# Kernel tuning notes

Measured on AMD Instinct MI355X. Metric: run time of the kernel, lower is better.

## Reference

```python
import jax, jax.numpy as jnp
import numpy as np

N_RAYS = 32768
N_SAMPLES = N_RAYS * 32  # 1,048,576
FDIM = 32
HID = 64
RGB_HID = 64
THRESHOLD = 1e-4  # early_termination_threshold


def setup_inputs() -> dict:
    key = jax.random.key(0)
    ks = jax.random.split(key, 12)
    # ragged per-ray sample counts (avg 32), adjusted so total is exactly N_SAMPLES
    rng = np.random.default_rng(0)
    counts = rng.integers(8, 57, size=N_RAYS)
    delta = int(N_SAMPLES - counts.sum())
    if delta >= 0:
        counts[:delta] += 1
    else:
        counts[:(-delta)] -= 1
    starts = np.concatenate([[0], np.cumsum(counts)[:-1]])
    packing_info = jnp.asarray(np.stack([starts, counts], axis=1), dtype=jnp.int32)
    ray_ids = jnp.asarray(np.repeat(np.arange(N_RAYS), counts), dtype=jnp.int32)

    pos = jax.random.uniform(ks[0], (N_SAMPLES, 3), minval=-1.0, maxval=1.0)
    dirs = jax.random.normal(ks[1], (N_SAMPLES, 3))
    dirs = dirs / jnp.linalg.norm(dirs, axis=1, keepdims=True)
    dt = jax.random.uniform(ks[2], (N_SAMPLES, 1), minval=0.0, maxval=0.01)
    packed_samples = jnp.concatenate([pos, dirs, dt], axis=1)

    def lin(k, fi, fo):
        return jax.random.normal(k, (fi, fo)) / np.sqrt(fi)

    return {
        "packed_samples": packed_samples,
        "packing_info": packing_info,
        "ray_ids": ray_ids,
        "w1": lin(ks[3], 3, HID), "b1": jnp.zeros(HID),
        "w2": lin(ks[4], HID, FDIM), "b2": jnp.zeros(FDIM),
        "w_sigma": lin(ks[5], FDIM, 1), "b_sigma": jnp.zeros(1),
        "w_rgb1": lin(ks[6], FDIM + 3, RGB_HID), "b_rgb1": jnp.zeros(RGB_HID),
        "w_rgb2": lin(ks[7], RGB_HID, 3), "b_rgb2": jnp.zeros(3),
        "bg_color": jnp.ones(3),
    }


def reference(packed_samples, packing_info, ray_ids, w1, b1, w2, b2,
              w_sigma, b_sigma, w_rgb1, b_rgb1, w_rgb2, b_rgb2, bg_color):
    pos = packed_samples[:, :3]
    dirs = packed_samples[:, 3:6]
    dt = packed_samples[:, 6]

    # feature_module
    feats = jax.nn.relu(pos @ w1 + b1) @ w2 + b2            # [N, FDIM]
    # sigma_decoder
    sigma = jax.nn.softplus(feats @ w_sigma + b_sigma)[:, 0]  # [N]

    # NerfWeights: per-ray transmittance T_i = exp(-sum_{j<i in ray} sigma_j*dt_j),
    # weight_i = T_i * (1 - exp(-sigma_i*dt_i)), zeroed once T drops below threshold.
    tau = sigma * dt
    c_excl = jnp.cumsum(tau) - tau                           # exclusive global cumsum
    seg_base = c_excl[packing_info[:, 0]]                    # cumsum before each ray's start
    T = jnp.exp(-(c_excl - seg_base[ray_ids]))
    alpha = 1.0 - jnp.exp(-tau)
    weights = jnp.where(T > THRESHOLD, T * alpha, 0.0)       # [N]

    # rgb_decoder (masked gather in torch is a perf trick; weight==0 kills masked rgbs)
    h = jax.nn.relu(jnp.concatenate([feats, dirs], axis=1) @ w_rgb1 + b_rgb1)
    rgbs = jax.nn.sigmoid(h @ w_rgb2 + b_rgb2)               # [N, 3]

    contrib = rgbs * weights[:, None]
    rendered = jax.ops.segment_sum(contrib, ray_ids, num_segments=N_RAYS)   # [n_rays,3]
    opac = jax.ops.segment_sum(weights, ray_ids, num_segments=N_RAYS)       # [n_rays]
    return rendered + bg_color * (1.0 - opac[:, None])
```

## Files before the change

kernel.cpp:

```cpp
#include <hip/hip_runtime.h>
#include <hip/hip_bf16.h>
#include <math.h>
#include <stdint.h>

#define N_RAYS    32768
#define N_SAMPLES (N_RAYS * 32)
#define N_TILES   (N_SAMPLES / 32)
#define THRESH 0.0001f
#define TBL_OFF  (16u * 1024u * 1024u)

#define R_A1   0
#define R_A2   2
#define R_R1A  6
#define R_R1B  10
#define R_AR2  12
#define R_AR2F 16
#define R_B2I  18
#define R_ARI  22
#define NREC   26

#define NWAVES 3072
#define NITER  11

typedef __attribute__((ext_vector_type(8)))  __bf16 bf16x8;
typedef __attribute__((ext_vector_type(16))) float  f32x16;
typedef float f4a __attribute__((ext_vector_type(4), aligned(4)));

union FragU  { __hip_bfloat162 h2[4]; uint32_t w[4]; bf16x8 v; };
union RecU   { bf16x8 v; uint4 u; };
union Rec16U { f32x16 v; uint4 u[4]; float f[16]; };

__device__ inline __hip_bfloat162 pk2(float lo, float hi) {
    float2 t; t.x = lo; t.y = hi;
    return __float22bfloat162_rn(t);
}

__device__ inline bf16x8 pack8(const float* vals) {
    FragU u;
    u.h2[0] = pk2(vals[0], vals[1]);
    u.h2[1] = pk2(vals[2], vals[3]);
    u.h2[2] = pk2(vals[4], vals[5]);
    u.h2[3] = pk2(vals[6], vals[7]);
    return u.v;
}

__device__ inline float rcp_fast(float x) {
    float r;
    asm("v_rcp_f32 %0, %1" : "=v"(r) : "v"(x));
    return r;
}
__device__ inline float sigmoid_fast(float x) { return rcp_fast(1.0f + __expf(-x)); }
__device__ inline float softplus_fast(float x) {
    const float e = __expf(-fabsf(x));
    return fmaxf(x, 0.0f) + __logf(1.0f + e);
}

template <int P>
__device__ inline bf16x8 packB_relu(f32x16 a) {
    FragU u;
    u.h2[0] = pk2(fmaxf(a[P+0],0.f), fmaxf(a[P+1],0.f));
    u.h2[1] = pk2(fmaxf(a[P+2],0.f), fmaxf(a[P+3],0.f));
    u.h2[2] = pk2(fmaxf(a[P+4],0.f), fmaxf(a[P+5],0.f));
    u.h2[3] = pk2(fmaxf(a[P+6],0.f), fmaxf(a[P+7],0.f));
    return u.v;
}
template <int P>
__device__ inline bf16x8 packB_relu2(f32x16 x, f32x16 y) {
    FragU u;
    u.h2[0] = pk2(fmaxf(x[P+0]+y[P+0],0.f), fmaxf(x[P+1]+y[P+1],0.f));
    u.h2[1] = pk2(fmaxf(x[P+2]+y[P+2],0.f), fmaxf(x[P+3]+y[P+3],0.f));
    u.h2[2] = pk2(fmaxf(x[P+4]+y[P+4],0.f), fmaxf(x[P+5]+y[P+5],0.f));
    u.h2[3] = pk2(fmaxf(x[P+6]+y[P+6],0.f), fmaxf(x[P+7]+y[P+7],0.f));
    return u.v;
}
template <int P>
__device__ inline bf16x8 packB_plain2(f32x16 x, f32x16 y) {
    FragU u;
    u.h2[0] = pk2(x[P+0]+y[P+0], x[P+1]+y[P+1]);
    u.h2[1] = pk2(x[P+2]+y[P+2], x[P+3]+y[P+3]);
    u.h2[2] = pk2(x[P+4]+y[P+4], x[P+5]+y[P+5]);
    u.h2[3] = pk2(x[P+6]+y[P+6], x[P+7]+y[P+7]);
    return u.v;
}

__global__ __launch_bounds__(256) void nerf_build_frags(
    const float* __restrict__ w1,  const float* __restrict__ b1,
    const float* __restrict__ w2,  const float* __restrict__ b2,
    const float* __restrict__ w_sigma, const float* __restrict__ b_sigma,
    const float* __restrict__ w_rgb1,  const float* __restrict__ b_rgb1,
    const float* __restrict__ w_rgb2,  const float* __restrict__ b_rgb2,
    uint4* __restrict__ tbl)
{
    const int wid  = threadIdx.x >> 6;
    const int lane = threadIdx.x & 63;
    const int m    = lane & 31;
    const int h    = lane >> 5;
    RecU rec;

    if (wid == 0) {
        #pragma unroll
        for (int t = 0; t < 2; ++t) {
            float v[8] = {0,0,0,0,0,0,0,0};
            if (h == 0) {
                const int j = 32*t + m;
                v[0] = w1[j]; v[1] = w1[64+j]; v[2] = w1[128+j]; v[3] = b1[j];
            }
            rec.v = pack8(v); tbl[(R_A1+t)*64 + lane] = rec.u;
        }
        #pragma unroll
        for (int c = 0; c < 4; ++c) {
            float v[8];
            #pragma unroll
            for (int q = 0; q < 8; ++q) {
                const int j = 16*c + (q&3) + 8*(q>>2) + 4*h;
                v[q] = w2[j*32 + m];
            }
            rec.v = pack8(v); tbl[(R_A2+c)*64 + lane] = rec.u;
        }
    } else if (wid == 1) {
        #pragma unroll
        for (int t = 0; t < 2; ++t)
            #pragma unroll
            for (int c = 0; c < 2; ++c) {
                float v[8];
                #pragma unroll
                for (int q = 0; q < 8; ++q) {
                    const int f = 16*c + (q&3) + 8*(q>>2) + 4*h;
                    v[q] = w_rgb1[f*64 + 32*t + m];
                }
                rec.v = pack8(v); tbl[(R_R1A+2*t+c)*64 + lane] = rec.u;
            }
        #pragma unroll
        for (int t = 0; t < 2; ++t) {
            float v[8] = {0,0,0,0,0,0,0,0};
            if (h == 1) {
                const int j = 32*t + m;
                v[0] = w_rgb1[32*64 + j]; v[1] = w_rgb1[33*64 + j];
                v[2] = w_rgb1[34*64 + j]; v[3] = b_rgb1[j];
            }
            rec.v = pack8(v); tbl[(R_R1B+t)*64 + lane] = rec.u;
        }
    } else if (wid == 2) {
        #pragma unroll
        for (int c = 0; c < 4; ++c) {
            float v[8];
            #pragma unroll
            for (int q = 0; q < 8; ++q) {
                const int hh = 16*c + (q&3) + 8*(q>>2) + 4*h;
                v[q] = (m < 3) ? w_rgb2[hh*3 + m] : 0.0f;
            }
            rec.v = pack8(v); tbl[(R_AR2+c)*64 + lane] = rec.u;
        }
        #pragma unroll
        for (int c = 0; c < 2; ++c) {
            float v[8];
            #pragma unroll
            for (int q = 0; q < 8; ++q) {
                const int f = 16*c + (q&3) + 8*(q>>2) + 4*h;
                v[q] = (m == 3) ? w_sigma[f] : 0.0f;
            }
            rec.v = pack8(v); tbl[(R_AR2F+c)*64 + lane] = rec.u;
        }
        Rec16U r16;
        #pragma unroll
        for (int i = 0; i < 4; ++i) {
            #pragma unroll
            for (int e = 0; e < 4; ++e) r16.f[4*i+e] = b2[e + 8*i + 4*h];
        }
        #pragma unroll
        for (int i = 0; i < 4; ++i) tbl[(R_B2I+i)*64 + lane] = r16.u[i];
        #pragma unroll
        for (int i = 0; i < 4; ++i) {
            #pragma unroll
            for (int e = 0; e < 4; ++e) {
                const int r = e + 8*i + 4*h;
                r16.f[4*i+e] = (r < 3) ? b_rgb2[r] : ((r == 3) ? b_sigma[0] : 0.0f);
            }
        }
        #pragma unroll
        for (int i = 0; i < 4; ++i) tbl[(R_ARI+i)*64 + lane] = r16.u[i];
    }
}

__global__ __launch_bounds__(256, 3) void nerf_mlp_mfma(
    const float* __restrict__ samples,
    const uint4* __restrict__ tbl,
    float4* __restrict__ out)
{
    __shared__ uint4 wlds[NREC * 64];

    for (int i = threadIdx.x; i < NREC * 64; i += 256) wlds[i] = tbl[i];
    __syncthreads();

    const int lane = threadIdx.x & 63;
    const int m32  = lane & 31;
    const int h    = lane >> 5;
    const int wgid = (blockIdx.x * blockDim.x + threadIdx.x) >> 6;

    const uint4* wl = &wlds[lane];
    #define LDW(rec) ({ RecU r_; r_.u = wl[(rec)*64]; r_.v; })

    f4a sa[2], sb[2];
    {
        const float* sp = samples + (size_t)(wgid * 32 + m32) * 7;
        sa[0] = *(const f4a*)sp;  sb[0] = *(const f4a*)(sp + 3);
    }

    const f32x16 zero16 = {0,0,0,0,0,0,0,0,0,0,0,0,0,0,0,0};

    #pragma unroll
    for (int u = 0; u < NITER; ++u) {
        const int cb = u & 1;
        const int nb = (u + 1) & 1;
        const int t  = wgid + u * NWAVES;
        if (u < NITER - 1) {
            int tn = wgid + (u + 1) * NWAVES;
            if (tn > N_TILES - 1) tn = N_TILES - 1;
            const float* sp = samples + (size_t)(tn * 32 + m32) * 7;
            sa[nb] = *(const f4a*)sp;  sb[nb] = *(const f4a*)(sp + 3);
        }

        FragU bin;
        bin.h2[0] = pk2(h ? sb[cb].x : sa[cb].x, h ? sb[cb].y : sa[cb].y);
        bin.h2[1] = pk2(h ? sb[cb].z : sa[cb].z, 1.0f);
        bin.w[2] = 0; bin.w[3] = 0;

        bf16x8 B2c[4];
        {
            f32x16 a0 = __builtin_amdgcn_mfma_f32_32x32x16_bf16(LDW(R_A1+0), bin.v, zero16, 0,0,0);
            f32x16 a1 = __builtin_amdgcn_mfma_f32_32x32x16_bf16(LDW(R_A1+1), bin.v, zero16, 0,0,0);
            B2c[0] = packB_relu<0>(a0);
            B2c[1] = packB_relu<8>(a0);
            B2c[2] = packB_relu<0>(a1);
            B2c[3] = packB_relu<8>(a1);
        }

        bf16x8 Bf0, Bf1;
        {
            Rec16U rc;
            #pragma unroll
            for (int i = 0; i < 4; ++i) rc.u[i] = wl[(R_B2I+i)*64];
            f32x16 u0, u1;
            u0 = __builtin_amdgcn_mfma_f32_32x32x16_bf16(LDW(R_A2+0), B2c[0], rc.v, 0,0,0);
            u1 = __builtin_amdgcn_mfma_f32_32x32x16_bf16(LDW(R_A2+2), B2c[2], zero16, 0,0,0);
            u0 = __builtin_amdgcn_mfma_f32_32x32x16_bf16(LDW(R_A2+1), B2c[1], u0, 0,0,0);
            u1 = __builtin_amdgcn_mfma_f32_32x32x16_bf16(LDW(R_A2+3), B2c[3], u1, 0,0,0);
            Bf0 = packB_plain2<0>(u0, u1);
            Bf1 = packB_plain2<8>(u0, u1);
        }

        bf16x8 Bh[4];
        {
            f32x16 p0, p1, q0, q1;
            q0 = __builtin_amdgcn_mfma_f32_32x32x16_bf16(LDW(R_R1B+0), bin.v, zero16, 0,0,0);
            q1 = __builtin_amdgcn_mfma_f32_32x32x16_bf16(LDW(R_R1B+1), bin.v, zero16, 0,0,0);
            p0 = __builtin_amdgcn_mfma_f32_32x32x16_bf16(LDW(R_R1A+0), Bf0, zero16, 0,0,0);
            p1 = __builtin_amdgcn_mfma_f32_32x32x16_bf16(LDW(R_R1A+2), Bf0, zero16, 0,0,0);
            p0 = __builtin_amdgcn_mfma_f32_32x32x16_bf16(LDW(R_R1A+1), Bf1, p0, 0,0,0);
            p1 = __builtin_amdgcn_mfma_f32_32x32x16_bf16(LDW(R_R1A+3), Bf1, p1, 0,0,0);
            Bh[0] = packB_relu2<0>(p0, q0);
            Bh[1] = packB_relu2<8>(p0, q0);
            Bh[2] = packB_relu2<0>(p1, q1);
            Bh[3] = packB_relu2<8>(p1, q1);
        }

        float ar0, ar1, ar2, ar3;
        {
            Rec16U rc;
            #pragma unroll
            for (int i = 0; i < 4; ++i) rc.u[i] = wl[(R_ARI+i)*64];
            f32x16 x, y, z;
            x = __builtin_amdgcn_mfma_f32_32x32x16_bf16(LDW(R_AR2F+0), Bf0, rc.v, 0,0,0);
            y = __builtin_amdgcn_mfma_f32_32x32x16_bf16(LDW(R_AR2+0), Bh[0], zero16, 0,0,0);
            z = __builtin_amdgcn_mfma_f32_32x32x16_bf16(LDW(R_AR2+2), Bh[2], zero16, 0,0,0);
            x = __builtin_amdgcn_mfma_f32_32x32x16_bf16(LDW(R_AR2F+1), Bf1, x, 0,0,0);
            y = __builtin_amdgcn_mfma_f32_32x32x16_bf16(LDW(R_AR2+1), Bh[1], y, 0,0,0);
            z = __builtin_amdgcn_mfma_f32_32x32x16_bf16(LDW(R_AR2+3), Bh[3], z, 0,0,0);
            ar0 = x[0] + y[0] + z[0];
            ar1 = x[1] + y[1] + z[1];
            ar2 = x[2] + y[2] + z[2];
            ar3 = x[3] + y[3] + z[3];
        }

        const float rr    = sigmoid_fast(ar0);
        const float gg    = sigmoid_fast(ar1);
        const float bb    = sigmoid_fast(ar2);
        const float sigma = softplus_fast(ar3);
        const float tau   = sigma * sb[cb].w;
        if (t < N_TILES && lane < 32)
            out[t * 32 + m32] = make_float4(tau, rr, gg, bb);
    }
    #undef LDW
}

__global__ __launch_bounds__(256) void nerf_render_kernel(
    const float4* __restrict__ smp,
    const int*    __restrict__ packing,
    const float*  __restrict__ bg,
    float*        __restrict__ out)
{
    const int gtid = blockIdx.x * blockDim.x + threadIdx.x;
    const int ray  = gtid >> 6;
    const int lane = threadIdx.x & 63;
    if (ray >= N_RAYS) return;

    const int start = packing[2 * ray];
    const int count = packing[2 * ray + 1];

    float tau = 0.0f, r = 0.0f, g = 0.0f, b = 0.0f;
    if (lane < count) {
        const float4 v = smp[start + lane];
        tau = v.x; r = v.y; g = v.z; b = v.w;
    }

    float incl = tau;
    #pragma unroll
    for (int off = 1; off < 64; off <<= 1) {
        const float v = __shfl_up(incl, off, 64);
        if (lane >= off) incl += v;
    }
    const float c_excl = incl - tau;

    const float T     = __expf(-c_excl);
    const float alpha = 1.0f - __expf(-tau);
    float w = (lane < count && T > THRESH) ? T * alpha : 0.0f;

    float cr = r * w, cg = g * w, cb = b * w;

    #pragma unroll
    for (int off = 32; off > 0; off >>= 1) {
        cr += __shfl_down(cr, off, 64);
        cg += __shfl_down(cg, off, 64);
        cb += __shfl_down(cb, off, 64);
        w  += __shfl_down(w,  off, 64);
    }

    if (lane == 0) {
        out[ray * 3 + 0] = cr + bg[0] * (1.0f - w);
        out[ray * 3 + 1] = cg + bg[1] * (1.0f - w);
        out[ray * 3 + 2] = cb + bg[2] * (1.0f - w);
    }
}

extern "C" void kernel_launch(void* const* d_in, const int* in_sizes, int n_in,
                              void* d_out, int out_size, void* d_ws, size_t ws_size,
                              hipStream_t stream) {
    const float* samples  = (const float*)d_in[0];
    const int*   packing  = (const int*)  d_in[1];
    const float* w1       = (const float*)d_in[3];
    const float* b1       = (const float*)d_in[4];
    const float* w2       = (const float*)d_in[5];
    const float* b2       = (const float*)d_in[6];
    const float* w_sigma  = (const float*)d_in[7];
    const float* b_sigma  = (const float*)d_in[8];
    const float* w_rgb1   = (const float*)d_in[9];
    const float* b_rgb1   = (const float*)d_in[10];
    const float* w_rgb2   = (const float*)d_in[11];
    const float* b_rgb2   = (const float*)d_in[12];
    const float* bg       = (const float*)d_in[13];

    float4* smp = (float4*)d_ws;
    uint4*  tbl = (uint4*)((char*)d_ws + TBL_OFF);
    float*  out = (float*)d_out;

    nerf_build_frags<<<1, 256, 0, stream>>>(
        w1, b1, w2, b2, w_sigma, b_sigma,
        w_rgb1, b_rgb1, w_rgb2, b_rgb2, tbl);

    nerf_mlp_mfma<<<768, 256, 0, stream>>>(samples, tbl, (float4*)smp);

    nerf_render_kernel<<<(N_RAYS * 64) / 256, 256, 0, stream>>>(smp, packing, bg, out);
}
```

Before: 49.92 us.

## Fuse MLP and volume rendering into one kernel with ray-grouped blocks

Merges the MFMA MLP kernel and the render kernel into a single kernel where each block handles 8 consecutive rays. It evaluates the MLP on their packed samples and keeps tau/rgb in LDS before the per-ray scan and reduction. This removes the 16 MB intermediate write/read through global memory and one kernel launch. In exchange it drops the persistent-wave software prefetch and the 3-wave occupancy hint, and relies on 8 rays never exceeding 464 samples. Blocks also now do ragged tile counts, which can leave some waves idle.

New measurement: 70.62 us. 41.5% more time.

```diff
diff --git a/kernel.cpp b/kernel.cpp
--- a/kernel.cpp
+++ b/kernel.cpp
@@ -5,9 +5,9 @@
 
 #define N_RAYS    32768
 #define N_SAMPLES (N_RAYS * 32)
-#define N_TILES   (N_SAMPLES / 32)
 #define THRESH 0.0001f
-#define TBL_OFF  (16u * 1024u * 1024u)
+#define RPB    8
+#define MAXS   464
 
 #define R_A1   0
 #define R_A2   2
@@ -18,9 +18,6 @@
 #define R_B2I  18
 #define R_ARI  22
 #define NREC   26
-
-#define NWAVES 3072
-#define NITER  11
 
 typedef __attribute__((ext_vector_type(8)))  __bf16 bf16x8;
 typedef __attribute__((ext_vector_type(16))) float  f32x16;
@@ -182,47 +179,47 @@
     }
 }
 
-__global__ __launch_bounds__(256, 3) void nerf_mlp_mfma(
+__global__ __launch_bounds__(256) void nerf_fused(
     const float* __restrict__ samples,
+    const int*   __restrict__ packing,
     const uint4* __restrict__ tbl,
-    float4* __restrict__ out)
+    const float* __restrict__ bg,
+    float*       __restrict__ out)
 {
-    __shared__ uint4 wlds[NREC * 64];
+    __shared__ uint4  wlds[NREC * 64];
+    __shared__ float4 obuf[MAXS];
 
     for (int i = threadIdx.x; i < NREC * 64; i += 256) wlds[i] = tbl[i];
-    __syncthreads();
 
     const int lane = threadIdx.x & 63;
     const int m32  = lane & 31;
     const int h    = lane >> 5;
-    const int wgid = (blockIdx.x * blockDim.x + threadIdx.x) >> 6;
+    const int wid  = threadIdx.x >> 6;
+    const int ray0 = blockIdx.x * RPB;
+
+    const int start0 = packing[2 * ray0];
+    int total = 0;
+    #pragma unroll
+    for (int i = 0; i < RPB; ++i) total += packing[2 * (ray0 + i) + 1];
+
+    __syncthreads();
 
     const uint4* wl = &wlds[lane];
     #define LDW(rec) ({ RecU r_; r_.u = wl[(rec)*64]; r_.v; })
 
-    f4a sa[2], sb[2];
-    {
-        const float* sp = samples + (size_t)(wgid * 32 + m32) * 7;
-        sa[0] = *(const f4a*)sp;  sb[0] = *(const f4a*)(sp + 3);
-    }
-
     const f32x16 zero16 = {0,0,0,0,0,0,0,0,0,0,0,0,0,0,0,0};
-
-    #pragma unroll
-    for (int u = 0; u < NITER; ++u) {
-        const int cb = u & 1;
-        const int nb = (u + 1) & 1;
-        const int t  = wgid + u * NWAVES;
-        if (u < NITER - 1) {
-            int tn = wgid + (u + 1) * NWAVES;
-            if (tn > N_TILES - 1) tn = N_TILES - 1;
-            const float* sp = samples + (size_t)(tn * 32 + m32) * 7;
-            sa[nb] = *(const f4a*)sp;  sb[nb] = *(const f4a*)(sp + 3);
-        }
+    const int ntiles = (total + 31) >> 5;
+
+    for (int t = wid; t < ntiles; t += 4) {
+        const int sidx  = 32 * t + m32;
+        const int cl    = (sidx < total) ? sidx : (total - 1);
+        const float* sp = samples + (size_t)(start0 + cl) * 7;
+        const f4a sa = *(const f4a*)sp;
+        const f4a sb = *(const f4a*)(sp + 3);
 
         FragU bin;
-        bin.h2[0] = pk2(h ? sb[cb].x : sa[cb].x, h ? sb[cb].y : sa[cb].y);
-        bin.h2[1] = pk2(h ? sb[cb].z : sa[cb].z, 1.0f);
+        bin.h2[0] = pk2(h ? sb.x : sa.x, h ? sb.y : sa.y);
+        bin.h2[1] = pk2(h ? sb.z : sa.z, 1.0f);
         bin.w[2] = 0; bin.w[3] = 0;
 
         bf16x8 B2c[4];
@@ -286,59 +283,53 @@
         const float gg    = sigmoid_fast(ar1);
         const float bb    = sigmoid_fast(ar2);
         const float sigma = softplus_fast(ar3);
-        const float tau   = sigma * sb[cb].w;
-        if (t < N_TILES && lane < 32)
-            out[t * 32 + m32] = make_float4(tau, rr, gg, bb);
+        const float tau   = sigma * sb.w;
+        if (lane < 32 && sidx < total)
+            obuf[sidx] = make_float4(tau, rr, gg, bb);
     }
     #undef LDW
-}
-
-__global__ __launch_bounds__(256) void nerf_render_kernel(
-    const float4* __restrict__ smp,
-    const int*    __restrict__ packing,
-    const float*  __restrict__ bg,
-    float*        __restrict__ out)
-{
-    const int gtid = blockIdx.x * blockDim.x + threadIdx.x;
-    const int ray  = gtid >> 6;
-    const int lane = threadIdx.x & 63;
-    if (ray >= N_RAYS) return;
-
-    const int start = packing[2 * ray];
-    const int count = packing[2 * ray + 1];
-
-    float tau = 0.0f, r = 0.0f, g = 0.0f, b = 0.0f;
-    if (lane < count) {
-        const float4 v = smp[start + lane];
-        tau = v.x; r = v.y; g = v.z; b = v.w;
-    }
-
-    float incl = tau;
+
+    __syncthreads();
+
+    const float bg0 = bg[0], bg1 = bg[1], bg2 = bg[2];
     #pragma unroll
-    for (int off = 1; off < 64; off <<= 1) {
-        const float v = __shfl_up(incl, off, 64);
-        if (lane >= off) incl += v;
-    }
-    const float c_excl = incl - tau;
-
-    const float T     = __expf(-c_excl);
-    const float alpha = 1.0f - __expf(-tau);
-    float w = (lane < count && T > THRESH) ? T * alpha : 0.0f;
-
-    float cr = r * w, cg = g * w, cb = b * w;
-
-    #pragma unroll
-    for (int off = 32; off > 0; off >>= 1) {
-        cr += __shfl_down(cr, off, 64);
-        cg += __shfl_down(cg, off, 64);
-        cb += __shfl_down(cb, off, 64);
-        w  += __shfl_down(w,  off, 64);
-    }
-
-    if (lane == 0) {
-        out[ray * 3 + 0] = cr + bg[0] * (1.0f - w);
-        out[ray * 3 + 1] = cg + bg[1] * (1.0f - w);
-        out[ray * 3 + 2] = cb + bg[2] * (1.0f - w);
+    for (int ri = 0; ri < 2; ++ri) {
+        const int ray   = ray0 + wid * 2 + ri;
+        const int rs    = packing[2 * ray] - start0;
+        const int count = packing[2 * ray + 1];
+
+        float tau = 0.0f, r = 0.0f, g = 0.0f, b = 0.0f;
+        if (lane < count) {
+            const float4 v = obuf[rs + lane];
+            tau = v.x; r = v.y; g = v.z; b = v.w;
+        }
+
+        float incl = tau;
+        #pragma unroll
+        for (int off = 1; off < 64; off <<= 1) {
+            const float v = __shfl_up(incl, off, 64);
+            if (lane >= off) incl += v;
+        }
+        const float c_excl = incl - tau;
+
+        const float T     = __expf(-c_excl);
+        const float alpha = 1.0f - __expf(-tau);
+        float w = (lane < count && T > THRESH) ? T * alpha : 0.0f;
+
+        float cr = r * w, cg = g * w, cb = b * w;
+        #pragma unroll
+        for (int off = 32; off > 0; off >>= 1) {
+            cr += __shfl_down(cr, off, 64);
+            cg += __shfl_down(cg, off, 64);
+            cb += __shfl_down(cb, off, 64);
+            w  += __shfl_down(w,  off, 64);
+        }
+
+        if (lane == 0) {
+            out[ray * 3 + 0] = cr + bg0 * (1.0f - w);
+            out[ray * 3 + 1] = cg + bg1 * (1.0f - w);
+            out[ray * 3 + 2] = cb + bg2 * (1.0f - w);
+        }
     }
 }
 
@@ -359,15 +350,12 @@
     const float* b_rgb2   = (const float*)d_in[12];
     const float* bg       = (const float*)d_in[13];
 
-    float4* smp = (float4*)d_ws;
-    uint4*  tbl = (uint4*)((char*)d_ws + TBL_OFF);
-    float*  out = (float*)d_out;
+    uint4* tbl = (uint4*)d_ws;
+    float* out = (float*)d_out;
 
     nerf_build_frags<<<1, 256, 0, stream>>>(
         w1, b1, w2, b2, w_sigma, b_sigma,
         w_rgb1, b_rgb1, w_rgb2, b_rgb2, tbl);
 
-    nerf_mlp_mfma<<<768, 256, 0, stream>>>(samples, tbl, (float4*)smp);
-
-    nerf_render_kernel<<<(N_RAYS * 64) / 256, 256, 0, stream>>>(smp, packing, bg, out);
-}
+    nerf_fused<<<N_RAYS / RPB, 256, 0, stream>>>(samples, packing, tbl, bg, out);
+}
```
